# Kernel optimization log

Measured on AMD Instinct MI355X. Metric: run time of the kernel, lower is better.

## Reference

```python
import jax, jax.numpy as jnp
import numpy as np

HID = 128
SCALE = np.sqrt(HID)


def _ln(x, g, b, eps=1e-5):
    m = jnp.mean(x, axis=-1, keepdims=True)
    v = jnp.mean((x - m) ** 2, axis=-1, keepdims=True)
    return (x - m) * jax.lax.rsqrt(v + eps) * g + b


def _attention(img, txt, Wi, bi, Wt, bt, g1, b1, Wq, bq, Wk, bk, Wv, bv, g2, b2, Wo, bo):
    # img: [..., S, image_dim], txt: [..., S, text_dim] -> [..., S, HID]
    c = img @ Wi.T + bi + txt @ Wt.T + bt
    c = _ln(c, g1, b1)
    q = c @ Wq.T + bq
    k = c @ Wk.T + bk
    v = c @ Wv.T + bv
    s = jnp.einsum('...qd,...kd->...qk', q, k) / (SCALE + 1e-8)
    a = jax.nn.softmax(s, axis=-1)
    a = a + 1e-10
    a = a / jnp.sum(a, axis=-1, keepdims=True)
    a = jnp.clip(a, 1e-7, 1.0)
    ctx = jnp.einsum('...qk,...kd->...qd', a, v)
    ctx = _ln(ctx, g2, b2)
    return ctx @ Wo.T + bo


def setup_inputs() -> dict:
    key = jax.random.key(0)
    ks = jax.random.split(key, 24)
    T, Q, DI, DT = 256, 64, 2048, 768

    def xavier(k, shape):
        fan_in, fan_out = shape[1], shape[0]
        lim = np.sqrt(6.0 / (fan_in + fan_out))
        return jax.random.uniform(k, shape, jnp.float32, -lim, lim)

    return {
        'support_images': jax.random.normal(ks[0], (T, 4, DI), jnp.float32),
        'support_texts': jax.random.normal(ks[1], (T, 4, DT), jnp.float32),
        'support_labels': jax.random.randint(ks[2], (T, 4), 0, 4, jnp.int64),
        'query_images': jax.random.normal(ks[3], (T, Q, DI), jnp.float32),
        'query_texts': jax.random.normal(ks[4], (T, Q, DT), jnp.float32),
        'Wi': xavier(ks[5], (HID, DI)), 'bi': jnp.zeros((HID,)),
        'Wt': xavier(ks[6], (HID, DT)), 'bt': jnp.zeros((HID,)),
        'g1': jnp.ones((HID,)), 'b1': jnp.zeros((HID,)),
        'Wq': xavier(ks[7], (HID, HID)), 'bq': jnp.zeros((HID,)),
        'Wk': xavier(ks[8], (HID, HID)), 'bk': jnp.zeros((HID,)),
        'Wv': xavier(ks[9], (HID, HID)), 'bv': jnp.zeros((HID,)),
        'g2': jnp.ones((HID,)), 'b2': jnp.zeros((HID,)),
        'Wo': xavier(ks[10], (HID, HID)), 'bo': jnp.zeros((HID,)),
    }


def reference(support_images, support_texts, support_labels, query_images, query_texts,
              Wi, bi, Wt, bt, g1, b1, Wq, bq, Wk, bk, Wv, bv, g2, b2, Wo, bo):
    p = (Wi, bi, Wt, bt, g1, b1, Wq, bq, Wk, bk, Wv, bv, g2, b2, Wo, bo)
    # Support: attention across the 4 support items of each task -> [T, 4, HID]
    support_feats = _attention(support_images, support_texts, *p)
    # Queries: source processes each query alone (seq len 1) -> add singleton seq axis
    qf = _attention(query_images[:, :, None, :], query_texts[:, :, None, :], *p)
    qf = qf[:, :, 0, :]  # [T, Q, HID]
    # Cosine-similarity prototype scoring (eps=1e-8 as in F.cosine_similarity)
    qn = qf / jnp.clip(jnp.linalg.norm(qf, axis=-1, keepdims=True), 1e-8, None)
    pn = support_feats / jnp.clip(jnp.linalg.norm(support_feats, axis=-1, keepdims=True), 1e-8, None)
    logits = jnp.einsum('tqd,tcd->tqc', qn, pn) * 10.0  # [T, Q, 4]
    return logits
```

## Files before the change

### kernel.cpp

```cpp
#include <hip/hip_runtime.h>

typedef __bf16 bf16_t;
typedef __attribute__((ext_vector_type(4))) __bf16 bf16x4;
typedef __attribute__((ext_vector_type(8))) __bf16 bf16x8;
typedef __attribute__((ext_vector_type(4))) float floatx4;

#define LN_EPS 1e-5f

#define K1_SA 40
#define K1_SB 40

__global__ __launch_bounds__(256) void k1_gemm(
    const float* __restrict__ qimg, const float* __restrict__ qtxt,
    const float* __restrict__ simg, const float* __restrict__ stxt,
    const float* __restrict__ Wi,   const float* __restrict__ Wt,
    const float* __restrict__ bi,   const float* __restrict__ bt,
    float* __restrict__ c_all)
{
    __shared__ bf16_t lA[64 * K1_SA];
    __shared__ bf16_t lB[128 * K1_SB];

    const int tid  = threadIdx.x;
    const int m0   = blockIdx.x * 64;
    const bool isq = (m0 < 16384);
    const int rb   = isq ? m0 : (m0 - 16384);
    const float* Aimg = isq ? qimg : simg;
    const float* Atxt = isq ? qtxt : stxt;

    const int wid  = tid >> 6;
    const int lane = tid & 63;
    const int quad = lane >> 4;
    const int l16  = lane & 15;
    const int wr   = wid >> 1;
    const int wc   = wid & 1;

    const int srow = tid >> 3;
    const int sc4  = tid & 7;

    floatx4 acc[2][4];
#pragma unroll
    for (int i = 0; i < 2; ++i)
#pragma unroll
        for (int j = 0; j < 4; ++j) acc[i][j] = (floatx4)0.f;

    for (int k0 = 0; k0 < 2816; k0 += 32) {
        const float* abase; const float* bbase; size_t lda, ldb;
        if (k0 < 2048) {
            abase = Aimg + (size_t)rb * 2048 + k0; lda = 2048;
            bbase = Wi + k0;                        ldb = 2048;
        } else {
            abase = Atxt + (size_t)rb * 768 + (k0 - 2048); lda = 768;
            bbase = Wt + (k0 - 2048);                       ldb = 768;
        }
        __syncthreads();
#pragma unroll
        for (int p = 0; p < 2; ++p) {
            int r = srow + p * 32;
            float4 v = *(const float4*)(abase + (size_t)r * lda + sc4 * 4);
            bf16x4 pk; pk.x = (bf16_t)v.x; pk.y = (bf16_t)v.y;
                       pk.z = (bf16_t)v.z; pk.w = (bf16_t)v.w;
            *(bf16x4*)&lA[r * K1_SA + sc4 * 4] = pk;
        }
#pragma unroll
        for (int p = 0; p < 4; ++p) {
            int r = srow + p * 32;
            float4 v = *(const float4*)(bbase + (size_t)r * ldb + sc4 * 4);
            bf16x4 pk; pk.x = (bf16_t)v.x; pk.y = (bf16_t)v.y;
                       pk.z = (bf16_t)v.z; pk.w = (bf16_t)v.w;
            *(bf16x4*)&lB[r * K1_SB + sc4 * 4] = pk;
        }
        __syncthreads();
        bf16x8 af[2], bfr[4];
#pragma unroll
        for (int mt = 0; mt < 2; ++mt)
            af[mt] = *(const bf16x8*)&lA[(wr * 32 + mt * 16 + l16) * K1_SA + quad * 8];
#pragma unroll
        for (int nt = 0; nt < 4; ++nt)
            bfr[nt] = *(const bf16x8*)&lB[(wc * 64 + nt * 16 + l16) * K1_SB + quad * 8];
#pragma unroll
        for (int mt = 0; mt < 2; ++mt)
#pragma unroll
            for (int nt = 0; nt < 4; ++nt)
                acc[mt][nt] = __builtin_amdgcn_mfma_f32_16x16x32_bf16(
                    af[mt], bfr[nt], acc[mt][nt], 0, 0, 0);
    }
#pragma unroll
    for (int nt = 0; nt < 4; ++nt) {
        int col = wc * 64 + nt * 16 + l16;
        float bias = bi[col] + bt[col];
#pragma unroll
        for (int mt = 0; mt < 2; ++mt)
#pragma unroll
            for (int r = 0; r < 4; ++r) {
                int row = wr * 32 + mt * 16 + quad * 4 + r;
                c_all[(size_t)(m0 + row) * 128 + col] = acc[mt][nt][r] + bias;
            }
    }
}

#define K2_ST 136

__global__ __launch_bounds__(256) void k2_query(
    const float* __restrict__ c_all,
    const float* __restrict__ Wv, const float* __restrict__ bv,
    const float* __restrict__ Wo, const float* __restrict__ bo,
    const float* __restrict__ g1, const float* __restrict__ b1,
    const float* __restrict__ g2, const float* __restrict__ b2,
    float* __restrict__ qn)
{
    __shared__ bf16_t tT[64 * K2_ST];
    __shared__ bf16_t tW[128 * K2_ST];

    const int tid  = threadIdx.x;
    const int wid  = tid >> 6;
    const int lane = tid & 63;
    const int quad = lane >> 4;
    const int l16  = lane & 15;
    const int t0   = blockIdx.x * 64;
    const int r0   = wid * 16;

    float bvr[8], g2r[8], b2r[8], bor[8];
#pragma unroll
    for (int nt = 0; nt < 8; ++nt) {
        int col = nt * 16 + l16;
        bvr[nt] = bv[col]; g2r[nt] = g2[col]; b2r[nt] = b2[col]; bor[nt] = bo[col];
    }
    const float g1l = g1[lane], g1h = g1[64 + lane];
    const float b1l = b1[lane], b1h = b1[64 + lane];

    for (int i = 0; i < 16; ++i) {
        int row = r0 + i;
        const float* src = c_all + (size_t)(t0 + row) * 128;
        float x0 = src[lane], x1 = src[64 + lane];
        float s = x0 + x1, q = x0 * x0 + x1 * x1;
#pragma unroll
        for (int m = 1; m < 64; m <<= 1) { s += __shfl_xor(s, m); q += __shfl_xor(q, m); }
        float mean = s * (1.f / 128.f);
        float var  = q * (1.f / 128.f) - mean * mean;
        float rs   = rsqrtf(var + LN_EPS);
        tT[row * K2_ST + lane]      = (bf16_t)((x0 - mean) * rs * g1l + b1l);
        tT[row * K2_ST + 64 + lane] = (bf16_t)((x1 - mean) * rs * g1h + b1h);
    }
#pragma unroll
    for (int i = 0; i < 16; ++i) {
        int idx = i * 1024 + tid * 4;
        int r = idx >> 7, cc = idx & 127;
        float4 v = *(const float4*)(Wv + idx);
        bf16x4 pk; pk.x = (bf16_t)v.x; pk.y = (bf16_t)v.y;
                   pk.z = (bf16_t)v.z; pk.w = (bf16_t)v.w;
        *(bf16x4*)&tW[r * K2_ST + cc] = pk;
    }
    __syncthreads();

    floatx4 acc[8];
#pragma unroll
    for (int nt = 0; nt < 8; ++nt) acc[nt] = (floatx4)0.f;
#pragma unroll
    for (int ks = 0; ks < 4; ++ks) {
        bf16x8 a = *(const bf16x8*)&tT[(r0 + l16) * K2_ST + ks * 32 + quad * 8];
#pragma unroll
        for (int nt = 0; nt < 8; ++nt) {
            bf16x8 b = *(const bf16x8*)&tW[(nt * 16 + l16) * K2_ST + ks * 32 + quad * 8];
            acc[nt] = __builtin_amdgcn_mfma_f32_16x16x32_bf16(a, b, acc[nt], 0, 0, 0);
        }
    }
#pragma unroll
    for (int nt = 0; nt < 8; ++nt)
#pragma unroll
        for (int r = 0; r < 4; ++r) acc[nt][r] += bvr[nt];

#pragma unroll
    for (int r = 0; r < 4; ++r) {
        float s = 0.f, q = 0.f;
#pragma unroll
        for (int nt = 0; nt < 8; ++nt) { float x = acc[nt][r]; s += x; q += x * x; }
#pragma unroll
        for (int m = 1; m < 16; m <<= 1) { s += __shfl_xor(s, m); q += __shfl_xor(q, m); }
        float mean = s * (1.f / 128.f);
        float var  = q * (1.f / 128.f) - mean * mean;
        float rs   = rsqrtf(var + LN_EPS);
        int row = r0 + quad * 4 + r;
#pragma unroll
        for (int nt = 0; nt < 8; ++nt) {
            float y = (acc[nt][r] - mean) * rs * g2r[nt] + b2r[nt];
            tT[row * K2_ST + nt * 16 + l16] = (bf16_t)y;
        }
    }
    __syncthreads();
#pragma unroll
    for (int i = 0; i < 16; ++i) {
        int idx = i * 1024 + tid * 4;
        int r = idx >> 7, cc = idx & 127;
        float4 v = *(const float4*)(Wo + idx);
        bf16x4 pk; pk.x = (bf16_t)v.x; pk.y = (bf16_t)v.y;
                   pk.z = (bf16_t)v.z; pk.w = (bf16_t)v.w;
        *(bf16x4*)&tW[r * K2_ST + cc] = pk;
    }
    __syncthreads();

#pragma unroll
    for (int nt = 0; nt < 8; ++nt) acc[nt] = (floatx4)0.f;
#pragma unroll
    for (int ks = 0; ks < 4; ++ks) {
        bf16x8 a = *(const bf16x8*)&tT[(r0 + l16) * K2_ST + ks * 32 + quad * 8];
#pragma unroll
        for (int nt = 0; nt < 8; ++nt) {
            bf16x8 b = *(const bf16x8*)&tW[(nt * 16 + l16) * K2_ST + ks * 32 + quad * 8];
            acc[nt] = __builtin_amdgcn_mfma_f32_16x16x32_bf16(a, b, acc[nt], 0, 0, 0);
        }
    }
#pragma unroll
    for (int r = 0; r < 4; ++r) {
        float q = 0.f;
#pragma unroll
        for (int nt = 0; nt < 8; ++nt) {
            float x = acc[nt][r] + bor[nt]; acc[nt][r] = x; q += x * x;
        }
#pragma unroll
        for (int m = 1; m < 16; m <<= 1) q += __shfl_xor(q, m);
        float inv = 1.f / fmaxf(sqrtf(q), 1e-8f);
        int row = t0 + r0 + quad * 4 + r;
#pragma unroll
        for (int nt = 0; nt < 8; ++nt)
            qn[(size_t)row * 128 + nt * 16 + l16] = acc[nt][r] * inv;
    }
}

__global__ __launch_bounds__(256) void k3_support(
    const float* __restrict__ c_all,
    const float* __restrict__ Wq, const float* __restrict__ bq,
    const float* __restrict__ Wk, const float* __restrict__ bk,
    const float* __restrict__ Wv, const float* __restrict__ bv,
    const float* __restrict__ Wo, const float* __restrict__ bo,
    const float* __restrict__ g1, const float* __restrict__ b1,
    const float* __restrict__ g2, const float* __restrict__ b2,
    float* __restrict__ pn)
{
    __shared__ float cs[4][128];
    __shared__ float qkv[3][4][128];
    __shared__ float att[4][4];
    __shared__ float ctx[4][128];

    const int tid  = threadIdx.x;
    const int wid  = tid >> 6;
    const int lane = tid & 63;
    const int task = blockIdx.x;

    {
        const float* src = c_all + (size_t)(16384 + task * 4 + wid) * 128;
        float x0 = src[lane], x1 = src[64 + lane];
        float s = x0 + x1, q = x0 * x0 + x1 * x1;
#pragma unroll
        for (int m = 1; m < 64; m <<= 1) { s += __shfl_xor(s, m); q += __shfl_xor(q, m); }
        float mean = s * (1.f / 128.f);
        float var  = q * (1.f / 128.f) - mean * mean;
        float rs   = rsqrtf(var + LN_EPS);
        cs[wid][lane]      = (x0 - mean) * rs * g1[lane] + b1[lane];
        cs[wid][64 + lane] = (x1 - mean) * rs * g1[64 + lane] + b1[64 + lane];
    }
    __syncthreads();
#pragma unroll
    for (int j = 0; j < 6; ++j) {
        int o = tid + j * 256;
        int wsel = o >> 9;
        int rem  = o & 511;
        int s = rem >> 7, n = rem & 127;
        const float* W = (wsel == 0) ? Wq : (wsel == 1) ? Wk : Wv;
        const float* B = (wsel == 0) ? bq : (wsel == 1) ? bk : bv;
        const float4* w4 = (const float4*)(W + n * 128);
        const float4* c4 = (const float4*)cs[s];
        float acc = 0.f;
#pragma unroll
        for (int k = 0; k < 32; ++k) {
            float4 a = c4[k], b = w4[k];
            acc += a.x * b.x + a.y * b.y + a.z * b.z + a.w * b.w;
        }
        qkv[wsel][s][n] = acc + B[n];
    }
    __syncthreads();
    if (tid < 16) {
        int i = tid >> 2, j = tid & 3;
        float acc = 0.f;
        for (int k = 0; k < 128; ++k) acc += qkv[0][i][k] * qkv[1][j][k];
        att[i][j] = acc * (float)(1.0 / (11.313708498984761 + 1e-8));
    }
    __syncthreads();
    if (tid < 4) {
        float s0 = att[tid][0], s1 = att[tid][1], s2 = att[tid][2], s3 = att[tid][3];
        float m = fmaxf(fmaxf(s0, s1), fmaxf(s2, s3));
        float e0 = expf(s0 - m), e1 = expf(s1 - m), e2 = expf(s2 - m), e3 = expf(s3 - m);
        float se = e0 + e1 + e2 + e3;
        float a0 = e0 / se + 1e-10f, a1 = e1 / se + 1e-10f;
        float a2 = e2 / se + 1e-10f, a3 = e3 / se + 1e-10f;
        float t = a0 + a1 + a2 + a3;
        att[tid][0] = fminf(fmaxf(a0 / t, 1e-7f), 1.f);
        att[tid][1] = fminf(fmaxf(a1 / t, 1e-7f), 1.f);
        att[tid][2] = fminf(fmaxf(a2 / t, 1e-7f), 1.f);
        att[tid][3] = fminf(fmaxf(a3 / t, 1e-7f), 1.f);
    }
    __syncthreads();
#pragma unroll
    for (int j = 0; j < 2; ++j) {
        int o = tid + j * 256;
        int s = o >> 7, n = o & 127;
        ctx[s][n] = att[s][0] * qkv[2][0][n] + att[s][1] * qkv[2][1][n]
                  + att[s][2] * qkv[2][2][n] + att[s][3] * qkv[2][3][n];
    }
    __syncthreads();
    {
        float x0 = ctx[wid][lane], x1 = ctx[wid][64 + lane];
        float s = x0 + x1, q = x0 * x0 + x1 * x1;
#pragma unroll
        for (int m = 1; m < 64; m <<= 1) { s += __shfl_xor(s, m); q += __shfl_xor(q, m); }
        float mean = s * (1.f / 128.f);
        float var  = q * (1.f / 128.f) - mean * mean;
        float rs   = rsqrtf(var + LN_EPS);
        cs[wid][lane]      = (x0 - mean) * rs * g2[lane] + b2[lane];
        cs[wid][64 + lane] = (x1 - mean) * rs * g2[64 + lane] + b2[64 + lane];
    }
    __syncthreads();
#pragma unroll
    for (int j = 0; j < 2; ++j) {
        int o = tid + j * 256;
        int s = o >> 7, n = o & 127;
        const float4* w4 = (const float4*)(Wo + n * 128);
        const float4* c4 = (const float4*)cs[s];
        float acc = 0.f;
#pragma unroll
        for (int k = 0; k < 32; ++k) {
            float4 a = c4[k], b = w4[k];
            acc += a.x * b.x + a.y * b.y + a.z * b.z + a.w * b.w;
        }
        ctx[s][n] = acc + bo[n];
    }
    __syncthreads();
    {
        float x0 = ctx[wid][lane], x1 = ctx[wid][64 + lane];
        float q = x0 * x0 + x1 * x1;
#pragma unroll
        for (int m = 1; m < 64; m <<= 1) q += __shfl_xor(q, m);
        float inv = 1.f / fmaxf(sqrtf(q), 1e-8f);
        float* dst = pn + (size_t)(task * 4 + wid) * 128;
        dst[lane]      = x0 * inv;
        dst[64 + lane] = x1 * inv;
    }
}

__global__ __launch_bounds__(256) void k4_logits(
    const float* __restrict__ qn, const float* __restrict__ pn,
    float* __restrict__ out)
{
    __shared__ float pl[4][128];
    const int tid  = threadIdx.x;
    const int task = blockIdx.x;
#pragma unroll
    for (int j = 0; j < 2; ++j) {
        int o = tid + j * 256;
        int cc = o >> 7, k = o & 127;
        pl[cc][k] = pn[(size_t)(task * 4 + cc) * 128 + k];
    }
    __syncthreads();
    const int qi = tid >> 2, cc = tid & 3;
    const float4* q4 = (const float4*)(qn + (size_t)(task * 64 + qi) * 128);
    const float4* p4 = (const float4*)pl[cc];
    float acc = 0.f;
#pragma unroll
    for (int k = 0; k < 32; ++k) {
        float4 a = q4[k], b = p4[k];
        acc += a.x * b.x + a.y * b.y + a.z * b.z + a.w * b.w;
    }
    out[(size_t)task * 256 + qi * 4 + cc] = acc * 10.f;
}

extern "C" void kernel_launch(void* const* d_in, const int* in_sizes, int n_in,
                              void* d_out, int out_size, void* d_ws, size_t ws_size,
                              hipStream_t stream)
{
    const float* simg = (const float*)d_in[0];
    const float* stxt = (const float*)d_in[1];
    const float* qimg = (const float*)d_in[3];
    const float* qtxt = (const float*)d_in[4];
    const float* Wi = (const float*)d_in[5];
    const float* bi = (const float*)d_in[6];
    const float* Wt = (const float*)d_in[7];
    const float* bt = (const float*)d_in[8];
    const float* g1 = (const float*)d_in[9];
    const float* b1 = (const float*)d_in[10];
    const float* Wq = (const float*)d_in[11];
    const float* bq = (const float*)d_in[12];
    const float* Wk = (const float*)d_in[13];
    const float* bk = (const float*)d_in[14];
    const float* Wv = (const float*)d_in[15];
    const float* bv = (const float*)d_in[16];
    const float* g2 = (const float*)d_in[17];
    const float* b2 = (const float*)d_in[18];
    const float* Wo = (const float*)d_in[19];
    const float* bo = (const float*)d_in[20];
    float* out = (float*)d_out;

    float* c_all = (float*)d_ws;
    float* qn    = c_all + (size_t)17408 * 128;
    float* pn    = qn    + (size_t)16384 * 128;

    k1_gemm<<<272, 256, 0, stream>>>(qimg, qtxt, simg, stxt, Wi, Wt, bi, bt, c_all);
    k2_query<<<256, 256, 0, stream>>>(c_all, Wv, bv, Wo, bo, g1, b1, g2, b2, qn);
    k3_support<<<256, 256, 0, stream>>>(c_all, Wq, bq, Wk, bk, Wv, bv, Wo, bo,
                                        g1, b1, g2, b2, pn);
    k4_logits<<<256, 256, 0, stream>>>(qn, pn, out);
}
```

Baseline: 380.3 us.

## Split-K the input projection GEMM with atomics and stage weights in LDS

The main projection GEMM is split four ways along K (grid 272x4). Each slice accumulates into a bias-initialized buffer with float atomics, and a new init kernel writes the bias. The k-step per iteration doubles to 64, and the LDS stride is widened to match. The goal is more blocks across the GPU's CUs, since the original 272 blocks underfill it. The support kernel now stages each weight matrix into LDS as bf16 instead of reading fp32 rows from global memory. The logits kernel tiles the query vectors into LDS. The trade-offs are atomic contention, an extra launch, nondeterministic summation order, and a bf16 rounding of the support weights.

```diff
diff --git a/kernel.cpp b/kernel.cpp
--- a/kernel.cpp
+++ b/kernel.cpp
@@ -7,14 +7,25 @@
 
 #define LN_EPS 1e-5f
 
-#define K1_SA 40
-#define K1_SB 40
+__global__ __launch_bounds__(256) void k0_init(
+    const float* __restrict__ bi, const float* __restrict__ bt,
+    float* __restrict__ c_all)
+{
+    int i = blockIdx.x * 256 + threadIdx.x;
+    int c4 = i & 31;
+    float4 a = ((const float4*)bi)[c4];
+    float4 b = ((const float4*)bt)[c4];
+    float4 v; v.x = a.x + b.x; v.y = a.y + b.y; v.z = a.z + b.z; v.w = a.w + b.w;
+    ((float4*)c_all)[i] = v;
+}
+
+#define K1_SA 72
+#define K1_SB 72
 
 __global__ __launch_bounds__(256) void k1_gemm(
     const float* __restrict__ qimg, const float* __restrict__ qtxt,
     const float* __restrict__ simg, const float* __restrict__ stxt,
     const float* __restrict__ Wi,   const float* __restrict__ Wt,
-    const float* __restrict__ bi,   const float* __restrict__ bt,
     float* __restrict__ c_all)
 {
     __shared__ bf16_t lA[64 * K1_SA];
@@ -22,6 +33,7 @@
 
     const int tid  = threadIdx.x;
     const int m0   = blockIdx.x * 64;
+    const int chnk = blockIdx.y;
     const bool isq = (m0 < 16384);
     const int rb   = isq ? m0 : (m0 - 16384);
     const float* Aimg = isq ? qimg : simg;
@@ -34,8 +46,7 @@
     const int wr   = wid >> 1;
     const int wc   = wid & 1;
 
-    const int srow = tid >> 3;
-    const int sc4  = tid & 7;
+    const int arow = tid >> 2, acol = (tid & 3) * 4;
 
     floatx4 acc[2][4];
 #pragma unroll
@@ -43,7 +54,8 @@
 #pragma unroll
         for (int j = 0; j < 4; ++j) acc[i][j] = (floatx4)0.f;
 
-    for (int k0 = 0; k0 < 2816; k0 += 32) {
+    for (int s = 0; s < 11; ++s) {
+        const int k0 = chnk * 704 + s * 64;
         const float* abase; const float* bbase; size_t lda, ldb;
         if (k0 < 2048) {
             abase = Aimg + (size_t)rb * 2048 + k0; lda = 2048;
@@ -53,47 +65,55 @@
             bbase = Wt + (k0 - 2048);                       ldb = 768;
         }
         __syncthreads();
-#pragma unroll
-        for (int p = 0; p < 2; ++p) {
-            int r = srow + p * 32;
-            float4 v = *(const float4*)(abase + (size_t)r * lda + sc4 * 4);
-            bf16x4 pk; pk.x = (bf16_t)v.x; pk.y = (bf16_t)v.y;
-                       pk.z = (bf16_t)v.z; pk.w = (bf16_t)v.w;
-            *(bf16x4*)&lA[r * K1_SA + sc4 * 4] = pk;
-        }
-#pragma unroll
-        for (int p = 0; p < 4; ++p) {
-            int r = srow + p * 32;
-            float4 v = *(const float4*)(bbase + (size_t)r * ldb + sc4 * 4);
-            bf16x4 pk; pk.x = (bf16_t)v.x; pk.y = (bf16_t)v.y;
-                       pk.z = (bf16_t)v.z; pk.w = (bf16_t)v.w;
-            *(bf16x4*)&lB[r * K1_SB + sc4 * 4] = pk;
+        {
+            const float* p = abase + (size_t)arow * lda + acol;
+#pragma unroll
+            for (int j = 0; j < 4; ++j) {
+                float4 v = *(const float4*)(p + 16 * j);
+                bf16x4 pk; pk.x = (bf16_t)v.x; pk.y = (bf16_t)v.y;
+                           pk.z = (bf16_t)v.z; pk.w = (bf16_t)v.w;
+                *(bf16x4*)&lA[arow * K1_SA + acol + 16 * j] = pk;
+            }
+        }
+#pragma unroll
+        for (int pp = 0; pp < 2; ++pp) {
+            int brow = pp * 64 + (tid >> 2);
+            const float* p = bbase + (size_t)brow * ldb + acol;
+#pragma unroll
+            for (int j = 0; j < 4; ++j) {
+                float4 v = *(const float4*)(p + 16 * j);
+                bf16x4 pk; pk.x = (bf16_t)v.x; pk.y = (bf16_t)v.y;
+                           pk.z = (bf16_t)v.z; pk.w = (bf16_t)v.w;
+                *(bf16x4*)&lB[brow * K1_SB + acol + 16 * j] = pk;
+            }
         }
         __syncthreads();
-        bf16x8 af[2], bfr[4];
-#pragma unroll
-        for (int mt = 0; mt < 2; ++mt)
-            af[mt] = *(const bf16x8*)&lA[(wr * 32 + mt * 16 + l16) * K1_SA + quad * 8];
-#pragma unroll
-        for (int nt = 0; nt < 4; ++nt)
-            bfr[nt] = *(const bf16x8*)&lB[(wc * 64 + nt * 16 + l16) * K1_SB + quad * 8];
-#pragma unroll
-        for (int mt = 0; mt < 2; ++mt)
+#pragma unroll
+        for (int ks = 0; ks < 2; ++ks) {
+            bf16x8 af[2], bfr[4];
+#pragma unroll
+            for (int mt = 0; mt < 2; ++mt)
+                af[mt] = *(const bf16x8*)&lA[(wr * 32 + mt * 16 + l16) * K1_SA + ks * 32 + quad * 8];
 #pragma unroll
             for (int nt = 0; nt < 4; ++nt)
-                acc[mt][nt] = __builtin_amdgcn_mfma_f32_16x16x32_bf16(
-                    af[mt], bfr[nt], acc[mt][nt], 0, 0, 0);
+                bfr[nt] = *(const bf16x8*)&lB[(wc * 64 + nt * 16 + l16) * K1_SB + ks * 32 + quad * 8];
+#pragma unroll
+            for (int mt = 0; mt < 2; ++mt)
+#pragma unroll
+                for (int nt = 0; nt < 4; ++nt)
+                    acc[mt][nt] = __builtin_amdgcn_mfma_f32_16x16x32_bf16(
+                        af[mt], bfr[nt], acc[mt][nt], 0, 0, 0);
+        }
     }
 #pragma unroll
     for (int nt = 0; nt < 4; ++nt) {
         int col = wc * 64 + nt * 16 + l16;
-        float bias = bi[col] + bt[col];
 #pragma unroll
         for (int mt = 0; mt < 2; ++mt)
 #pragma unroll
             for (int r = 0; r < 4; ++r) {
                 int row = wr * 32 + mt * 16 + quad * 4 + r;
-                c_all[(size_t)(m0 + row) * 128 + col] = acc[mt][nt][r] + bias;
+                unsafeAtomicAdd(&c_all[(size_t)(m0 + row) * 128 + col], acc[mt][nt][r]);
             }
     }
 }
@@ -236,10 +256,11 @@
     const float* __restrict__ g2, const float* __restrict__ b2,
     float* __restrict__ pn)
 {
-    __shared__ float cs[4][128];
-    __shared__ float qkv[3][4][128];
-    __shared__ float att[4][4];
-    __shared__ float ctx[4][128];
+    __shared__ float  cs[4][128];
+    __shared__ bf16_t tW[128 * K2_ST];
+    __shared__ float  qkv[3][4][128];
+    __shared__ float  att[4][4];
+    __shared__ float  ctx[4][128];
 
     const int tid  = threadIdx.x;
     const int wid  = tid >> 6;
@@ -258,30 +279,50 @@
         cs[wid][lane]      = (x0 - mean) * rs * g1[lane] + b1[lane];
         cs[wid][64 + lane] = (x1 - mean) * rs * g1[64 + lane] + b1[64 + lane];
     }
-    __syncthreads();
-#pragma unroll
-    for (int j = 0; j < 6; ++j) {
-        int o = tid + j * 256;
-        int wsel = o >> 9;
-        int rem  = o & 511;
-        int s = rem >> 7, n = rem & 127;
-        const float* W = (wsel == 0) ? Wq : (wsel == 1) ? Wk : Wv;
-        const float* B = (wsel == 0) ? bq : (wsel == 1) ? bk : bv;
-        const float4* w4 = (const float4*)(W + n * 128);
-        const float4* c4 = (const float4*)cs[s];
-        float acc = 0.f;
-#pragma unroll
-        for (int k = 0; k < 32; ++k) {
-            float4 a = c4[k], b = w4[k];
-            acc += a.x * b.x + a.y * b.y + a.z * b.z + a.w * b.w;
-        }
-        qkv[wsel][s][n] = acc + B[n];
+
+    const float* Ws[3] = { Wq, Wk, Wv };
+    const float* Bs[3] = { bq, bk, bv };
+    for (int w = 0; w < 3; ++w) {
+        __syncthreads();
+#pragma unroll
+        for (int i = 0; i < 16; ++i) {
+            int idx = i * 1024 + tid * 4;
+            int r = idx >> 7, cc = idx & 127;
+            float4 v = *(const float4*)(Ws[w] + idx);
+            bf16x4 pk; pk.x = (bf16_t)v.x; pk.y = (bf16_t)v.y;
+                       pk.z = (bf16_t)v.z; pk.w = (bf16_t)v.w;
+            *(bf16x4*)&tW[r * K2_ST + cc] = pk;
+        }
+        __syncthreads();
+#pragma unroll
+        for (int j = 0; j < 2; ++j) {
+            int o = tid + j * 256;
+            int s = o >> 7, n = o & 127;
+            const float4* c4 = (const float4*)cs[s];
+            float acc = 0.f;
+#pragma unroll
+            for (int k8 = 0; k8 < 16; ++k8) {
+                bf16x8 wv = *(const bf16x8*)&tW[n * K2_ST + k8 * 8];
+                float4 a0 = c4[k8 * 2], a1 = c4[k8 * 2 + 1];
+                acc += a0.x * (float)wv[0] + a0.y * (float)wv[1]
+                     + a0.z * (float)wv[2] + a0.w * (float)wv[3]
+                     + a1.x * (float)wv[4] + a1.y * (float)wv[5]
+                     + a1.z * (float)wv[6] + a1.w * (float)wv[7];
+            }
+            qkv[w][s][n] = acc + Bs[w][n];
+        }
     }
     __syncthreads();
     if (tid < 16) {
         int i = tid >> 2, j = tid & 3;
+        const float4* qv = (const float4*)qkv[0][i];
+        const float4* kv = (const float4*)qkv[1][j];
         float acc = 0.f;
-        for (int k = 0; k < 128; ++k) acc += qkv[0][i][k] * qkv[1][j][k];
+#pragma unroll
+        for (int k = 0; k < 32; ++k) {
+            float4 a = qv[k], b = kv[k];
+            acc += a.x * b.x + a.y * b.y + a.z * b.z + a.w * b.w;
+        }
         att[i][j] = acc * (float)(1.0 / (11.313708498984761 + 1e-8));
     }
     __syncthreads();
@@ -320,16 +361,29 @@
     }
     __syncthreads();
 #pragma unroll
+    for (int i = 0; i < 16; ++i) {
+        int idx = i * 1024 + tid * 4;
+        int r = idx >> 7, cc = idx & 127;
+        float4 v = *(const float4*)(Wo + idx);
+        bf16x4 pk; pk.x = (bf16_t)v.x; pk.y = (bf16_t)v.y;
+                   pk.z = (bf16_t)v.z; pk.w = (bf16_t)v.w;
+        *(bf16x4*)&tW[r * K2_ST + cc] = pk;
+    }
+    __syncthreads();
+#pragma unroll
     for (int j = 0; j < 2; ++j) {
         int o = tid + j * 256;
         int s = o >> 7, n = o & 127;
-        const float4* w4 = (const float4*)(Wo + n * 128);
         const float4* c4 = (const float4*)cs[s];
         float acc = 0.f;
 #pragma unroll
-        for (int k = 0; k < 32; ++k) {
-            float4 a = c4[k], b = w4[k];
-            acc += a.x * b.x + a.y * b.y + a.z * b.z + a.w * b.w;
+        for (int k8 = 0; k8 < 16; ++k8) {
+            bf16x8 wv = *(const bf16x8*)&tW[n * K2_ST + k8 * 8];
+            float4 a0 = c4[k8 * 2], a1 = c4[k8 * 2 + 1];
+            acc += a0.x * (float)wv[0] + a0.y * (float)wv[1]
+                 + a0.z * (float)wv[2] + a0.w * (float)wv[3]
+                 + a1.x * (float)wv[4] + a1.y * (float)wv[5]
+                 + a1.z * (float)wv[6] + a1.w * (float)wv[7];
         }
         ctx[s][n] = acc + bo[n];
     }
@@ -350,19 +404,24 @@
     const float* __restrict__ qn, const float* __restrict__ pn,
     float* __restrict__ out)
 {
-    __shared__ float pl[4][128];
+    __shared__ float qs[64][132];
+    __shared__ float ps[4][132];
     const int tid  = threadIdx.x;
     const int task = blockIdx.x;
 #pragma unroll
-    for (int j = 0; j < 2; ++j) {
-        int o = tid + j * 256;
-        int cc = o >> 7, k = o & 127;
-        pl[cc][k] = pn[(size_t)(task * 4 + cc) * 128 + k];
+    for (int j = 0; j < 8; ++j) {
+        int i = tid + 256 * j;
+        int r = i >> 5, c = (i & 31) * 4;
+        *(float4*)&qs[r][c] = *(const float4*)(qn + ((size_t)task * 64 + r) * 128 + c);
+    }
+    if (tid < 128) {
+        int r = tid >> 5, c = (tid & 31) * 4;
+        *(float4*)&ps[r][c] = *(const float4*)(pn + ((size_t)task * 4 + r) * 128 + c);
     }
     __syncthreads();
     const int qi = tid >> 2, cc = tid & 3;
-    const float4* q4 = (const float4*)(qn + (size_t)(task * 64 + qi) * 128);
-    const float4* p4 = (const float4*)pl[cc];
+    const float4* q4 = (const float4*)qs[qi];
+    const float4* p4 = (const float4*)ps[cc];
     float acc = 0.f;
 #pragma unroll
     for (int k = 0; k < 32; ++k) {
@@ -402,7 +461,8 @@
     float* qn    = c_all + (size_t)17408 * 128;
     float* pn    = qn    + (size_t)16384 * 128;
 
-    k1_gemm<<<272, 256, 0, stream>>>(qimg, qtxt, simg, stxt, Wi, Wt, bi, bt, c_all);
+    k0_init<<<2176, 256, 0, stream>>>(bi, bt, c_all);
+    k1_gemm<<<dim3(272, 4), 256, 0, stream>>>(qimg, qtxt, simg, stxt, Wi, Wt, c_all);
     k2_query<<<256, 256, 0, stream>>>(c_all, Wv, bv, Wo, bo, g1, b1, g2, b2, qn);
     k3_support<<<256, 256, 0, stream>>>(c_all, Wq, bq, Wk, bk, Wv, bv, Wo, bo,
                                         g1, b1, g2, b2, pn);
```

New measurement: 384.8 us. Within noise of the previous version (+1.2%).
